# Optimization experiments

Measured on AMD Instinct MI355X. Metric: run time of the kernel, lower is better.

The kernel has to match this reference:

```python
import jax, jax.numpy as jnp
import numpy as np

Q = 10        # icosahedral diamonds
M = 128       # 2**dggrid_level
L = Q * M * M # 163840 icosahedral points
KS = 9        # kernel_size / knn neighbors


def setup_inputs() -> dict:
    key = jax.random.key(0)
    k1, k2, k3, k4 = jax.random.split(key, 4)
    b, c, h, w = 1, 128, 256, 512
    x = jax.random.normal(k1, (b, c, h, w), dtype=jnp.float32)
    codeskmin = jax.random.randint(k2, (L, KS), 0, h * w, dtype=jnp.int32)
    att_w = jax.random.normal(k3, (KS, 2, KS), dtype=jnp.float32) * 0.1
    att_b = jnp.zeros((KS,), dtype=jnp.float32)
    depth_w = jax.random.normal(k4, (c, KS), dtype=jnp.float32) * 0.1
    depth_b = jnp.zeros((c,), dtype=jnp.float32)
    gamma = jnp.ones((c,), dtype=jnp.float32)
    beta = jnp.zeros((c,), dtype=jnp.float32)
    return {"x": x, "codeskmin": codeskmin, "att_w": att_w, "att_b": att_b,
            "depth_w": depth_w, "depth_b": depth_b, "gamma": gamma, "beta": beta}


def reference(x, codeskmin, att_w, att_b, depth_w, depth_b, gamma, beta):
    b, c, h, w = x.shape
    xf = x.reshape(b, c, h * w)
    # KNN gather: (b, c, L, KS)
    xe = xf[:, :, codeskmin]
    # --- SpatialAttentionModule_v1 ---
    avg = jnp.mean(xe, axis=1)           # (b, L, KS)
    mx = jnp.max(xe, axis=1)             # (b, L, KS)
    feat = jnp.stack([avg, mx], axis=1)  # (b, 2, L, KS)
    # Conv2d(2 -> KS, kernel (1,KS), no pad): reduces neighbor axis fully
    att = jnp.einsum('bilk,oik->bol', feat, att_w) + att_b[None, :, None]  # (b, KS, L)
    att = jax.nn.sigmoid(att)
    att = att.transpose(0, 2, 1)[:, None, :, :]  # (b, 1, L, KS)
    xe = att * xe + xe
    # --- depthwise conv over neighbor axis ---
    out = jnp.einsum('bclk,ck->bcl', xe, depth_w) + depth_b[None, :, None]  # (b, c, L)
    # rearrange 'b c (q h w) -> (b q) c h w'
    out = out.reshape(b, c, Q, M, M).transpose(0, 2, 1, 3, 4).reshape(b * Q, c, M, M)
    # BatchNorm (training-mode batch stats)
    mean = jnp.mean(out, axis=(0, 2, 3), keepdims=True)
    var = jnp.var(out, axis=(0, 2, 3), keepdims=True)
    out = (out - mean) * jax.lax.rsqrt(var + 1e-5)
    out = out * gamma[None, :, None, None] + beta[None, :, None, None]
    # Swish
    out = out * jax.nn.sigmoid(out)
    return out
```

## Files before the change

### kernel.cpp

```cpp
#include <hip/hip_runtime.h>
#include <hip/hip_bf16.h>

#define HW 131072
#define NCH 128
#define KS 9
#define L_TOTAL 163840
#define NGRP 8
#define LPB 128

typedef float        f32x2 __attribute__((ext_vector_type(2)));
typedef float        f32x4 __attribute__((ext_vector_type(4)));
typedef unsigned int u32x2 __attribute__((ext_vector_type(2)));
typedef unsigned int u32x4 __attribute__((ext_vector_type(4)));

static __device__ __forceinline__ float bflo(unsigned int p) { return __uint_as_float(p << 16); }
static __device__ __forceinline__ float bfhi(unsigned int p) { return __uint_as_float(p & 0xffff0000u); }
static __device__ __forceinline__ unsigned short f2bf(float f) {
    unsigned int x = __float_as_uint(f);
    return (unsigned short)((x + 0x7fffu + ((x >> 16) & 1u)) >> 16);
}
static __device__ __forceinline__ unsigned int pack2(float a, float b) {
    return (unsigned int)f2bf(a) | ((unsigned int)f2bf(b) << 16);
}

__global__ __launch_bounds__(256) void transpose_x_kernel(
    const f32x2* __restrict__ xf,
    unsigned int* __restrict__ xT,
    float2* __restrict__ meanmaxP)
{
    __shared__ unsigned short tile[128 * 128];
    __shared__ float ps[4][128];
    __shared__ float pm[4][128];
    const int tid = threadIdx.x;
    const int lane = tid & 63;
    const int wave = tid >> 6;
    const int p0 = blockIdx.x * 128;
    const int pa = 2 * lane, pb = 2 * lane + 1;

    float s0 = 0.f, s1 = 0.f;
    float m0 = -3.4e38f, m1 = -3.4e38f;
    #pragma unroll 8
    for (int it = 0; it < 32; ++it) {
        int c = wave + (it << 2);
        f32x2 v = __builtin_nontemporal_load(&xf[(long)c * (HW / 2) + (p0 >> 1) + lane]);
        tile[pa * 128 + ((c + 2 * pa) & 127)] = f2bf(v.x);
        tile[pb * 128 + ((c + 2 * pb) & 127)] = f2bf(v.y);
        s0 += v.x; s1 += v.y;
        m0 = fmaxf(m0, v.x); m1 = fmaxf(m1, v.y);
    }
    ps[wave][pa] = s0; ps[wave][pb] = s1;
    pm[wave][pa] = m0; pm[wave][pb] = m1;
    __syncthreads();

    #pragma unroll 8
    for (int it = 0; it < 32; ++it) {
        int p = wave + (it << 2);
        int colr = (2 * lane + 2 * p) & 127;
        unsigned int d = *reinterpret_cast<const unsigned int*>(&tile[p * 128 + colr]);
        xT[((long)(lane >> 3) * HW + (p0 + p)) * 8 + (lane & 7)] = d;
    }
    if (tid < 128) {
        float s = ps[0][tid] + ps[1][tid] + ps[2][tid] + ps[3][tid];
        float m = fmaxf(fmaxf(pm[0][tid], pm[1][tid]), fmaxf(pm[2][tid], pm[3][tid]));
        meanmaxP[p0 + tid] = make_float2(s * 0.0078125f, m);
    }
}

__global__ __launch_bounds__(256) void mult_kernel(
    const float2* __restrict__ meanmaxP,
    const int* __restrict__ cks,
    const float* __restrict__ att_w,
    const float* __restrict__ att_b,
    unsigned int* __restrict__ rec)
{
    __shared__ float attw[162];
    __shared__ float attb[12];
    __shared__ int lcks[64 * 12];
    const int tid = threadIdx.x;
    const int base_l = blockIdx.x * 64;

    if (tid < 162) attw[tid] = att_w[tid];
    if (tid < KS) attb[tid] = att_b[tid];
    for (int j = tid; j < 64 * KS; j += 256) {
        const int lj = j / KS;
        lcks[lj * 12 + (j - lj * KS)] = cks[(long)base_l * KS + j];
    }
    __syncthreads();

    const int l_local = tid >> 2;
    const int sub = tid & 3;
    if (sub < 3) {
        float mean[KS], mx[KS];
        #pragma unroll
        for (int k = 0; k < KS; ++k) {
            float2 mm = meanmaxP[lcks[l_local * 12 + k]];
            mean[k] = mm.x; mx[k] = mm.y;
        }
        #pragma unroll
        for (int oo = 0; oo < 3; ++oo) {
            int o = sub * 3 + oo;
            float logit = attb[o];
            #pragma unroll
            for (int k = 0; k < KS; ++k) {
                logit = fmaf(mean[k], attw[o * 18 + k], logit);
                logit = fmaf(mx[k],   attw[o * 18 + 9 + k], logit);
            }
            float sig = 1.0f / (1.0f + __expf(-logit));
            unsigned int u = (unsigned int)(sig * 32768.0f + 0.5f);
            if (u > 32767u) u = 32767u;
            rec[(long)(base_l + l_local) * 12 + o] =
                (unsigned int)lcks[l_local * 12 + o] | (u << 17);
        }
    }
}

__global__ __launch_bounds__(256, 4) void gather_kernel(
    const unsigned int* __restrict__ xT,
    const unsigned int* __restrict__ rec,
    const float* __restrict__ depth_w,
    const float* __restrict__ depth_b,
    unsigned int* __restrict__ ybuf,
    float* __restrict__ gsum, float* __restrict__ gsq)
{
    __shared__ float dwl[KS][16];
    __shared__ float dbl[16];
    __shared__ float redx[4][4][8];

    const int tid  = threadIdx.x;
    const int lane = tid & 63;
    const int wave = tid >> 6;
    const int g      = blockIdx.x & 7;
    const int base_l = (blockIdx.x >> 3) * LPB;
    const int qt = lane & 3;
    const int lq = lane >> 2;

    if (tid < 144) {
        int k = tid >> 4, ch = tid & 15;
        dwl[k][ch] = depth_w[(g * 16 + ch) * KS + k];
    }
    if (tid < 16) dbl[tid] = depth_b[g * 16 + tid];
    __syncthreads();

    f32x2 dw[KS][2];
    #pragma unroll
    for (int k = 0; k < KS; ++k) {
        f32x4 t = *(const f32x4*)&dwl[k][qt * 4];
        dw[k][0].x = t.x; dw[k][0].y = t.y;
        dw[k][1].x = t.z; dw[k][1].y = t.w;
    }
    f32x2 db01, db23;
    {
        f32x4 t = *(const f32x4*)&dbl[qt * 4];
        db01.x = t.x; db01.y = t.y; db23.x = t.z; db23.y = t.w;
    }

    const unsigned int* slab  = xT   + ((size_t)g << 20);
    unsigned int*       yslab = ybuf + (size_t)g * (L_TOTAL * 8);

    f32x2 sum01 = {0.f, 0.f}, sum23 = {0.f, 0.f};
    f32x2 sq01  = {0.f, 0.f}, sq23  = {0.f, 0.f};

    #pragma unroll
    for (int b = 0; b < 2; ++b) {
        const int lloc = wave * 32 + b * 16 + lq;
        const unsigned int* rp = rec + (size_t)(base_l + lloc) * 12;
        const u32x4 r0 = __builtin_nontemporal_load((const u32x4*)rp);
        const u32x4 r1 = __builtin_nontemporal_load((const u32x4*)(rp + 4));
        const unsigned int r8 = __builtin_nontemporal_load(rp + 8);
        const unsigned int rr[KS] = {r0.x, r0.y, r0.z, r0.w,
                                     r1.x, r1.y, r1.z, r1.w, r8};

        u32x2 pv[KS];
        #pragma unroll
        for (int k = 0; k < KS; ++k)
            pv[k] = *(const u32x2*)(slab + ((rr[k] & 0x1FFFFu) << 3) + (qt << 1));

        f32x2 acc01 = db01, acc23 = db23;
        #pragma unroll
        for (int k = 0; k < KS; ++k) {
            const float mk = fmaf((float)(rr[k] >> 17), 3.0517578125e-5f, 1.0f);
            f32x2 mk2; mk2.x = mk; mk2.y = mk;
            f32x2 xa; xa.x = bflo(pv[k].x); xa.y = bfhi(pv[k].x);
            f32x2 xb; xb.x = bflo(pv[k].y); xb.y = bfhi(pv[k].y);
            acc01 = __builtin_elementwise_fma(xa * mk2, dw[k][0], acc01);
            acc23 = __builtin_elementwise_fma(xb * mk2, dw[k][1], acc23);
        }

        u32x2 o;
        o.x = pack2(acc01.x, acc01.y);
        o.y = pack2(acc23.x, acc23.y);
        *(u32x2*)(yslab + (size_t)(base_l + lloc) * 8 + (qt << 1)) = o;

        sum01 += acc01; sum23 += acc23;
        sq01 = __builtin_elementwise_fma(acc01, acc01, sq01);
        sq23 = __builtin_elementwise_fma(acc23, acc23, sq23);
    }

    #pragma unroll
    for (int s = 4; s <= 32; s <<= 1) {
        sum01.x += __shfl_xor(sum01.x, s);
        sum01.y += __shfl_xor(sum01.y, s);
        sum23.x += __shfl_xor(sum23.x, s);
        sum23.y += __shfl_xor(sum23.y, s);
        sq01.x  += __shfl_xor(sq01.x,  s);
        sq01.y  += __shfl_xor(sq01.y,  s);
        sq23.x  += __shfl_xor(sq23.x,  s);
        sq23.y  += __shfl_xor(sq23.y,  s);
    }
    if (lane < 4) {
        float* rw = &redx[wave][lane][0];
        rw[0] = sum01.x; rw[1] = sum01.y; rw[2] = sum23.x; rw[3] = sum23.y;
        rw[4] = sq01.x;  rw[5] = sq01.y;  rw[6] = sq23.x;  rw[7] = sq23.y;
    }
    __syncthreads();
    if (tid < 32) {
        const int q = tid >> 2, qq = tid & 3;
        float s = redx[0][qq][q] + redx[1][qq][q] + redx[2][qq][q] + redx[3][qq][q];
        const int ch = g * 16 + qq * 4 + (q & 3);
        float* dst = (q >= 4) ? gsq : gsum;
        atomicAdd(&dst[ch], s);
    }
}

__global__ __launch_bounds__(256) void finalize_kernel(
    const unsigned int* __restrict__ ybuf,
    const float* __restrict__ gsum, const float* __restrict__ gsq,
    const float* __restrict__ gamma, const float* __restrict__ beta,
    float* __restrict__ out)
{
    __shared__ unsigned short tile[128 * 130];
    const int tid = threadIdx.x;
    const int lane = tid & 63;
    const int wave = tid >> 6;
    const int q = blockIdx.x >> 7;
    const int r0 = (blockIdx.x & 127) * 128;
    const int gg = lane >> 3, dd = lane & 7;
    const int c0 = gg * 16 + 2 * dd, c1 = c0 + 1;

    const long lbase = (long)q * 16384 + r0;
    #pragma unroll 8
    for (int it = 0; it < 32; ++it) {
        int r = wave + (it << 2);
        unsigned int u = __builtin_nontemporal_load(
            &ybuf[((long)gg * L_TOTAL + lbase + r) * 8 + dd]);
        tile[c0 * 130 + r] = (unsigned short)(u & 0xffffu);
        tile[c1 * 130 + r] = (unsigned short)(u >> 16);
    }
    __syncthreads();

    const float invN = 1.0f / (float)L_TOTAL;
    #pragma unroll 4
    for (int it = 0; it < 32; ++it) {
        int c = wave + (it << 2);
        float m = gsum[c] * invN;
        float var = gsq[c] * invN - m * m;
        float sc = gamma[c] * rsqrtf(var + 1e-5f);
        float sh = beta[c] - m * sc;
        unsigned int d = *reinterpret_cast<const unsigned int*>(&tile[c * 130 + 2 * lane]);
        float z0 = fmaf(bflo(d), sc, sh);
        float z1 = fmaf(bfhi(d), sc, sh);
        f32x2 v;
        v.x = z0 / (1.0f + __expf(-z0));
        v.y = z1 / (1.0f + __expf(-z1));
        *(f32x2*)&out[((long)(q * NCH + c) << 14) + r0 + 2 * lane] = v;
    }
}

extern "C" void kernel_launch(void* const* d_in, const int* in_sizes, int n_in,
                              void* d_out, int out_size, void* d_ws, size_t ws_size,
                              hipStream_t stream) {
    const f32x2* x_f2  = (const f32x2*)d_in[0];
    const int* cks     = (const int*)d_in[1];
    const float* aw    = (const float*)d_in[2];
    const float* ab    = (const float*)d_in[3];
    const float* dw    = (const float*)d_in[4];
    const float* db    = (const float*)d_in[5];
    const float* gm    = (const float*)d_in[6];
    const float* bt    = (const float*)d_in[7];

    char* ws = (char*)d_ws;
    unsigned int* xT   = (unsigned int*)ws;
    float2* meanmaxP   = (float2*)(ws + 33554432);
    unsigned int* ybuf = (unsigned int*)(ws + 34603008);
    unsigned int* rec  = (unsigned int*)(ws + 76546048);
    float* gsum        = (float*)(ws + 84410368);
    float* gsq         = gsum + NCH;

    hipMemsetAsync(gsum, 0, 2 * NCH * sizeof(float), stream);

    transpose_x_kernel<<<HW / 128, 256, 0, stream>>>(x_f2, xT, meanmaxP);
    mult_kernel<<<L_TOTAL / 64, 256, 0, stream>>>(meanmaxP, cks, aw, ab, rec);
    gather_kernel<<<(L_TOTAL / LPB) * NGRP, 256, 0, stream>>>(
        xT, rec, dw, db, ybuf, gsum, gsq);
    finalize_kernel<<<1280, 256, 0, stream>>>(
        ybuf, gsum, gsq, gm, bt, (float*)d_out);
}
```

Before: 300.3 us.

## Store gather output channel-major and stream it in finalize without LDS transpose

The gather kernel now has each thread handle two adjacent points (LPB doubled) and writes its bf16 results in a channel-major layout, packing the two points of one channel into a single word. Because of that layout, the finalize kernel can give each block one channel and one diamond, read 16-byte vectors contiguously and write contiguous fp32 output. This drops the shared-memory transpose and its barrier from finalize. In exchange, the gather stores become narrower and more strided across four channel rows, register pressure rises with two accumulator sets per thread, and the gather grid has half as many blocks.

```diff
diff --git a/kernel.cpp b/kernel.cpp
--- a/kernel.cpp
+++ b/kernel.cpp
@@ -6,7 +6,7 @@
 #define KS 9
 #define L_TOTAL 163840
 #define NGRP 8
-#define LPB 128
+#define LPB 256
 
 typedef float        f32x2 __attribute__((ext_vector_type(2)));
 typedef float        f32x4 __attribute__((ext_vector_type(4)));
@@ -154,46 +154,64 @@
         db01.x = t.x; db01.y = t.y; db23.x = t.z; db23.y = t.w;
     }
 
-    const unsigned int* slab  = xT   + ((size_t)g << 20);
-    unsigned int*       yslab = ybuf + (size_t)g * (L_TOTAL * 8);
+    const unsigned int* slab = xT + ((size_t)g << 20);
+    const int LH = L_TOTAL / 2;
+    unsigned int* yb = ybuf + (size_t)(g * 16 + qt * 4) * LH + (base_l >> 1);
 
     f32x2 sum01 = {0.f, 0.f}, sum23 = {0.f, 0.f};
     f32x2 sq01  = {0.f, 0.f}, sq23  = {0.f, 0.f};
 
     #pragma unroll
     for (int b = 0; b < 2; ++b) {
-        const int lloc = wave * 32 + b * 16 + lq;
-        const unsigned int* rp = rec + (size_t)(base_l + lloc) * 12;
-        const u32x4 r0 = __builtin_nontemporal_load((const u32x4*)rp);
-        const u32x4 r1 = __builtin_nontemporal_load((const u32x4*)(rp + 4));
-        const unsigned int r8 = __builtin_nontemporal_load(rp + 8);
-        const unsigned int rr[KS] = {r0.x, r0.y, r0.z, r0.w,
-                                     r1.x, r1.y, r1.z, r1.w, r8};
-
-        u32x2 pv[KS];
+        const int lw = wave * 64 + b * 32 + 2 * lq;
+        const unsigned int* rp = rec + (size_t)(base_l + lw) * 12;
+        const u32x4 a0 = __builtin_nontemporal_load((const u32x4*)rp);
+        const u32x4 a1 = __builtin_nontemporal_load((const u32x4*)(rp + 4));
+        const unsigned int a8 = __builtin_nontemporal_load(rp + 8);
+        const u32x4 c0 = __builtin_nontemporal_load((const u32x4*)(rp + 12));
+        const u32x4 c1 = __builtin_nontemporal_load((const u32x4*)(rp + 16));
+        const unsigned int c8 = __builtin_nontemporal_load(rp + 20);
+        const unsigned int rA[KS] = {a0.x, a0.y, a0.z, a0.w,
+                                     a1.x, a1.y, a1.z, a1.w, a8};
+        const unsigned int rB[KS] = {c0.x, c0.y, c0.z, c0.w,
+                                     c1.x, c1.y, c1.z, c1.w, c8};
+
+        u32x2 pA[KS], pB[KS];
         #pragma unroll
         for (int k = 0; k < KS; ++k)
-            pv[k] = *(const u32x2*)(slab + ((rr[k] & 0x1FFFFu) << 3) + (qt << 1));
-
-        f32x2 acc01 = db01, acc23 = db23;
+            pA[k] = *(const u32x2*)(slab + ((rA[k] & 0x1FFFFu) << 3) + (qt << 1));
+        #pragma unroll
+        for (int k = 0; k < KS; ++k)
+            pB[k] = *(const u32x2*)(slab + ((rB[k] & 0x1FFFFu) << 3) + (qt << 1));
+
+        f32x2 aA01 = db01, aA23 = db23, aB01 = db01, aB23 = db23;
         #pragma unroll
         for (int k = 0; k < KS; ++k) {
-            const float mk = fmaf((float)(rr[k] >> 17), 3.0517578125e-5f, 1.0f);
-            f32x2 mk2; mk2.x = mk; mk2.y = mk;
-            f32x2 xa; xa.x = bflo(pv[k].x); xa.y = bfhi(pv[k].x);
-            f32x2 xb; xb.x = bflo(pv[k].y); xb.y = bfhi(pv[k].y);
-            acc01 = __builtin_elementwise_fma(xa * mk2, dw[k][0], acc01);
-            acc23 = __builtin_elementwise_fma(xb * mk2, dw[k][1], acc23);
+            const float mA = fmaf((float)(rA[k] >> 17), 3.0517578125e-5f, 1.0f);
+            f32x2 mA2; mA2.x = mA; mA2.y = mA;
+            f32x2 xa; xa.x = bflo(pA[k].x); xa.y = bfhi(pA[k].x);
+            f32x2 xb; xb.x = bflo(pA[k].y); xb.y = bfhi(pA[k].y);
+            aA01 = __builtin_elementwise_fma(xa * mA2, dw[k][0], aA01);
+            aA23 = __builtin_elementwise_fma(xb * mA2, dw[k][1], aA23);
+            const float mB = fmaf((float)(rB[k] >> 17), 3.0517578125e-5f, 1.0f);
+            f32x2 mB2; mB2.x = mB; mB2.y = mB;
+            f32x2 ya; ya.x = bflo(pB[k].x); ya.y = bfhi(pB[k].x);
+            f32x2 ybv; ybv.x = bflo(pB[k].y); ybv.y = bfhi(pB[k].y);
+            aB01 = __builtin_elementwise_fma(ya * mB2, dw[k][0], aB01);
+            aB23 = __builtin_elementwise_fma(ybv * mB2, dw[k][1], aB23);
         }
 
-        u32x2 o;
-        o.x = pack2(acc01.x, acc01.y);
-        o.y = pack2(acc23.x, acc23.y);
-        *(u32x2*)(yslab + (size_t)(base_l + lloc) * 8 + (qt << 1)) = o;
-
-        sum01 += acc01; sum23 += acc23;
-        sq01 = __builtin_elementwise_fma(acc01, acc01, sq01);
-        sq23 = __builtin_elementwise_fma(acc23, acc23, sq23);
+        const int pi = wave * 32 + b * 16 + lq;
+        yb[0 * LH + pi] = pack2(aA01.x, aB01.x);
+        yb[1 * LH + pi] = pack2(aA01.y, aB01.y);
+        yb[2 * LH + pi] = pack2(aA23.x, aB23.x);
+        yb[3 * LH + pi] = pack2(aA23.y, aB23.y);
+
+        sum01 += aA01 + aB01; sum23 += aA23 + aB23;
+        sq01 = __builtin_elementwise_fma(aA01, aA01, sq01);
+        sq01 = __builtin_elementwise_fma(aB01, aB01, sq01);
+        sq23 = __builtin_elementwise_fma(aA23, aA23, sq23);
+        sq23 = __builtin_elementwise_fma(aB23, aB23, sq23);
     }
 
     #pragma unroll
@@ -223,46 +241,40 @@
 }
 
 __global__ __launch_bounds__(256) void finalize_kernel(
-    const unsigned int* __restrict__ ybuf,
+    const u32x4* __restrict__ ybuf,
     const float* __restrict__ gsum, const float* __restrict__ gsq,
     const float* __restrict__ gamma, const float* __restrict__ beta,
     float* __restrict__ out)
 {
-    __shared__ unsigned short tile[128 * 130];
+    const int q = blockIdx.x >> 7;
+    const int c = blockIdx.x & 127;
     const int tid = threadIdx.x;
-    const int lane = tid & 63;
-    const int wave = tid >> 6;
-    const int q = blockIdx.x >> 7;
-    const int r0 = (blockIdx.x & 127) * 128;
-    const int gg = lane >> 3, dd = lane & 7;
-    const int c0 = gg * 16 + 2 * dd, c1 = c0 + 1;
-
-    const long lbase = (long)q * 16384 + r0;
-    #pragma unroll 8
-    for (int it = 0; it < 32; ++it) {
-        int r = wave + (it << 2);
-        unsigned int u = __builtin_nontemporal_load(
-            &ybuf[((long)gg * L_TOTAL + lbase + r) * 8 + dd]);
-        tile[c0 * 130 + r] = (unsigned short)(u & 0xffffu);
-        tile[c1 * 130 + r] = (unsigned short)(u >> 16);
-    }
-    __syncthreads();
 
     const float invN = 1.0f / (float)L_TOTAL;
-    #pragma unroll 4
-    for (int it = 0; it < 32; ++it) {
-        int c = wave + (it << 2);
-        float m = gsum[c] * invN;
-        float var = gsq[c] * invN - m * m;
-        float sc = gamma[c] * rsqrtf(var + 1e-5f);
-        float sh = beta[c] - m * sc;
-        unsigned int d = *reinterpret_cast<const unsigned int*>(&tile[c * 130 + 2 * lane]);
-        float z0 = fmaf(bflo(d), sc, sh);
-        float z1 = fmaf(bfhi(d), sc, sh);
-        f32x2 v;
-        v.x = z0 / (1.0f + __expf(-z0));
-        v.y = z1 / (1.0f + __expf(-z1));
-        *(f32x2*)&out[((long)(q * NCH + c) << 14) + r0 + 2 * lane] = v;
+    const float m = gsum[c] * invN;
+    const float var = gsq[c] * invN - m * m;
+    const float sc = gamma[c] * rsqrtf(var + 1e-5f);
+    const float sh = beta[c] - m * sc;
+
+    const u32x4* src = ybuf + (size_t)c * (L_TOTAL / 8) + (size_t)q * 2048;
+    float* dst = out + ((size_t)(q * NCH + c) << 14);
+
+    #pragma unroll 2
+    for (int it = 0; it < 8; ++it) {
+        const int i = it * 256 + tid;
+        const u32x4 v = src[i];
+        f32x4 o0, o1;
+        float z;
+        z = fmaf(bflo(v.x), sc, sh); o0.x = z / (1.0f + __expf(-z));
+        z = fmaf(bfhi(v.x), sc, sh); o0.y = z / (1.0f + __expf(-z));
+        z = fmaf(bflo(v.y), sc, sh); o0.z = z / (1.0f + __expf(-z));
+        z = fmaf(bfhi(v.y), sc, sh); o0.w = z / (1.0f + __expf(-z));
+        z = fmaf(bflo(v.z), sc, sh); o1.x = z / (1.0f + __expf(-z));
+        z = fmaf(bfhi(v.z), sc, sh); o1.y = z / (1.0f + __expf(-z));
+        z = fmaf(bflo(v.w), sc, sh); o1.z = z / (1.0f + __expf(-z));
+        z = fmaf(bfhi(v.w), sc, sh); o1.w = z / (1.0f + __expf(-z));
+        *(f32x4*)&dst[i * 8 + 0] = o0;
+        *(f32x4*)&dst[i * 8 + 4] = o1;
     }
 }
 
@@ -293,5 +305,5 @@
     gather_kernel<<<(L_TOTAL / LPB) * NGRP, 256, 0, stream>>>(
         xT, rec, dw, db, ybuf, gsum, gsq);
     finalize_kernel<<<1280, 256, 0, stream>>>(
-        ybuf, gsum, gsq, gm, bt, (float*)d_out);
-}
+        (const u32x4*)ybuf, gsum, gsq, gm, bt, (float*)d_out);
+}
```

New measurement: 307.0 us. 1.02x slower.
